# Performance work log

Measured on AMD Instinct MI355X. Metric: run time of the kernel, lower is better.

Reference implementation:

```python
import jax, jax.numpy as jnp
import numpy as np

B, S, L, D, C_ENC, H = 8, 4096, 77, 1280, 2048, 20
DH = D // H          # 64
SCALE = DH ** -0.5


def setup_inputs() -> dict:
    key = jax.random.key(0)
    ks = jax.random.split(key, 8)
    return {
        "hidden_states": jax.random.normal(ks[0], (B, S, D), jnp.float32),
        "encoder_hidden_states": jax.random.normal(ks[1], (B, L, C_ENC), jnp.float32),
        "region_state": jax.random.uniform(ks[2], (B, S, L), jnp.float32),
        "Wq": jax.random.normal(ks[3], (D, D), jnp.float32) * 0.02,
        "Wk": jax.random.normal(ks[4], (C_ENC, D), jnp.float32) * 0.02,
        "Wv": jax.random.normal(ks[5], (C_ENC, D), jnp.float32) * 0.02,
        "Wo": jax.random.normal(ks[6], (D, D), jnp.float32) * 0.02,
        "bo": jnp.zeros((D,), jnp.float32),
        "sigma": jnp.ones((1,), jnp.float32) * 14.6,
    }


def reference(hidden_states, encoder_hidden_states, region_state, Wq, Wk, Wv, Wo, bo, sigma):
    # QKV projections (dense GEMMs)
    q = (hidden_states @ Wq).reshape(B, S, H, DH)            # [B,S,H,dh]
    k = (encoder_hidden_states @ Wk).reshape(B, L, H, DH)    # [B,L,H,dh]
    v = (encoder_hidden_states @ Wv).reshape(B, L, H, DH)
    # scaled attention scores (baddbmm with beta=0 == plain scaled matmul)
    scores = jnp.einsum('bshd,blhd->bhsl', q, k) * SCALE      # [B,H,S,L]
    # region-prompt bias: weight_func(w, sigma, qk) = w * log(1 + 0.1*sigma) * qk.max()
    # repeat_interleave over heads == broadcast over the head axis
    bias = region_state * (jnp.log1p(sigma[0] * 0.1) * scores.max())  # [B,S,L]
    scores = scores + bias[:, None, :, :]
    probs = jax.nn.softmax(scores, axis=-1)
    out = jnp.einsum('bhsl,blhd->bshd', probs, v).reshape(B, S, D)
    # output projection (to_out[0]); to_out[1] is dropout (identity at eval)
    return out @ Wo + bo
```

## Files before the change

### kernel.cpp

```cpp
#include <hip/hip_runtime.h>
#include <hip/hip_bf16.h>
#include <math.h>

#define NB 8
#define NS 4096
#define NL 77
#define NLP 80
#define NLPV 96
#define ND 1280
#define NC 2048
#define NH 20
#define NDH 64
#define QK_SCALE 0.125f

typedef __attribute__((ext_vector_type(4))) float f32x4;
typedef __attribute__((ext_vector_type(8))) short bf16x8;

static __device__ __forceinline__ void gload_lds16(const void* g, void* l) {
  __builtin_amdgcn_global_load_lds(
      (const __attribute__((address_space(1))) void*)g,
      (__attribute__((address_space(3))) void*)l, 16, 0, 0);
}

#define BAR() do { asm volatile("" ::: "memory"); __builtin_amdgcn_s_barrier(); asm volatile("" ::: "memory"); } while (0)
#define LGKM0() asm volatile("s_waitcnt lgkmcnt(0)" ::: "memory")

__global__ void cvt_bf16_kern(const float* __restrict__ in,
                              __hip_bfloat16* __restrict__ out, long n)
{
  long i = ((long)blockIdx.x * blockDim.x + threadIdx.x) * 4;
  long stride = (long)gridDim.x * blockDim.x * 4;
  for (; i < n; i += stride) {
    float4 v = *reinterpret_cast<const float4*>(in + i);
    union { __hip_bfloat16 h[4]; ushort4 u; } r;
    r.h[0] = __float2bfloat16(v.x);
    r.h[1] = __float2bfloat16(v.y);
    r.h[2] = __float2bfloat16(v.z);
    r.h[3] = __float2bfloat16(v.w);
    *reinterpret_cast<ushort4*>(out + i) = r.u;
  }
}

__global__ void transpose_bf16_kern(const float* __restrict__ in,
                                    __hip_bfloat16* __restrict__ out,
                                    int rows, int cols)
{
  __shared__ float t[32][33];
  int c0 = blockIdx.x * 32, r0 = blockIdx.y * 32;
  int tx = threadIdx.x, ty = threadIdx.y;
  for (int i = ty; i < 32; i += 8) {
    int r = r0 + i, c = c0 + tx;
    t[i][tx] = (r < rows && c < cols) ? in[(long)r * cols + c] : 0.f;
  }
  __syncthreads();
  for (int i = ty; i < 32; i += 8) {
    int oc = c0 + i, orr = r0 + tx;
    if (oc < cols && orr < rows)
      out[(long)oc * rows + orr] = __float2bfloat16(t[tx][i]);
  }
}

__global__ __launch_bounds__(256)
void gemm_bt_kern(const __hip_bfloat16* __restrict__ A,
                  const __hip_bfloat16* __restrict__ Bt,
                  void* __restrict__ C, const float* __restrict__ bias,
                  int M, int N, int K, int mode)
{
  __shared__ __align__(16) __hip_bfloat16 As[128 * 32];
  __shared__ __align__(16) __hip_bfloat16 Bs[128 * 32];
  const int t = threadIdx.x;
  const int lane = t & 63;
  const int w = t >> 6;
  const int wm = w >> 1, wn = w & 1;
  const int lr = lane & 15, hi = lane >> 4, lk = hi * 8;
  const long m0 = (long)blockIdx.x * 128;
  const long n0 = (long)blockIdx.y * 128;

  f32x4 acc[4][4];
#pragma unroll
  for (int mi = 0; mi < 4; ++mi)
#pragma unroll
    for (int ni = 0; ni < 4; ++ni) acc[mi][ni] = {0.f, 0.f, 0.f, 0.f};

  for (int k0 = 0; k0 < K; k0 += 32) {
    __syncthreads();
#pragma unroll
    for (int rnd = 0; rnd < 2; ++rnd) {
      int idx = rnd * 256 + t;
      int row = idx >> 2, kpp = (idx & 3) * 8;
      long arow = m0 + row; if (arow >= M) arow = M - 1;
      gload_lds16(A + arow * K + k0 + kpp, (void*)(As + idx * 8));
      long brow = n0 + row;
      gload_lds16(Bt + brow * K + k0 + kpp, (void*)(Bs + idx * 8));
    }
    __syncthreads();

    bf16x8 af[4], bfr[4];
#pragma unroll
    for (int i = 0; i < 4; ++i) {
      af[i]  = *reinterpret_cast<const bf16x8*>(As + (wm * 64 + i * 16 + lr) * 32 + lk);
      bfr[i] = *reinterpret_cast<const bf16x8*>(Bs + (wn * 64 + i * 16 + lr) * 32 + lk);
    }
#pragma unroll
    for (int mi = 0; mi < 4; ++mi)
#pragma unroll
      for (int ni = 0; ni < 4; ++ni)
        acc[mi][ni] = __builtin_amdgcn_mfma_f32_16x16x32_bf16(af[mi], bfr[ni], acc[mi][ni], 0, 0, 0);
  }

#pragma unroll
  for (int mi = 0; mi < 4; ++mi) {
#pragma unroll
    for (int r = 0; r < 4; ++r) {
      long row = m0 + wm * 64 + mi * 16 + hi * 4 + r;
      if (row < M) {
#pragma unroll
        for (int ni = 0; ni < 4; ++ni) {
          long col = n0 + wn * 64 + ni * 16 + lr;
          if (mode == 0)
            ((__hip_bfloat16*)C)[row * N + col] = __float2bfloat16(acc[mi][ni][r]);
          else
            ((float*)C)[row * N + col] = acc[mi][ni][r] + bias[col];
        }
      }
    }
  }
}

__global__ __launch_bounds__(256, 2)
void gemm_qmax_kern(const __hip_bfloat16* __restrict__ A,
                    const __hip_bfloat16* __restrict__ Bt,
                    __hip_bfloat16* __restrict__ C,
                    const __hip_bfloat16* __restrict__ kp,
                    float* __restrict__ bmax,
                    int M, int N, int K)
{
  __shared__ __align__(16) __hip_bfloat16 sm[32768];
  char* smc = (char*)sm;

  const int t = threadIdx.x, lane = t & 63, w = t >> 6;
  const int wm = w >> 1, wn = w & 1;
  const int lr = lane & 15, hi = lane >> 4;
  const int sw = lr & 7;

  int nwg = gridDim.x;
  int cpx = nwg >> 3;
  int swz = (blockIdx.x & 7) * cpx + (blockIdx.x >> 3);
  int nxt = N >> 7;
  int mt = swz / nxt, ntile = swz - mt * nxt;
  const long m0 = (long)mt * 128, n0 = (long)ntile * 128;

  const int srow  = t >> 3;
  const int skoff = ((t & 7) ^ (srow & 7)) * 8;
  const int sdst  = t * 16;

  f32x4 acc[4][4];
#pragma unroll
  for (int mi = 0; mi < 4; ++mi)
#pragma unroll
    for (int ni = 0; ni < 4; ++ni) acc[mi][ni] = {0.f, 0.f, 0.f, 0.f};

  auto stageA = [&](int b, int kt) {
#pragma unroll
    for (int c = 0; c < 4; ++c)
      gload_lds16(A + (m0 + c * 32 + srow) * (long)K + kt * 64 + skoff,
                  (void*)(smc + b * 16384 + c * 4096 + sdst));
  };
  auto stageB = [&](int b, int kt) {
#pragma unroll
    for (int c = 0; c < 4; ++c)
      gload_lds16(Bt + (n0 + c * 32 + srow) * (long)K + kt * 64 + skoff,
                  (void*)(smc + 32768 + b * 16384 + c * 4096 + sdst));
  };

  const int NT = K >> 6;
  stageA(0, 0); stageB(0, 0);
  stageA(1, 1); stageB(1, 1);
  asm volatile("s_waitcnt vmcnt(8)" ::: "memory");
  BAR();

  for (int t2 = 0; t2 < NT; ++t2) {
    const int b = t2 & 1;
    const char* pa = smc + b * 16384;
    const char* pb = smc + 32768 + b * 16384;
    const bool pf = (t2 + 2 < NT);

    bf16x8 af[4][2], bfr[4][2];
#pragma unroll
    for (int mi = 0; mi < 4; ++mi) {
      int row = wm * 64 + mi * 16 + lr;
#pragma unroll
      for (int kk = 0; kk < 2; ++kk)
        af[mi][kk] = *reinterpret_cast<const bf16x8*>(
            pa + row * 128 + ((((kk * 4 + hi) ^ sw)) << 4));
    }
#pragma unroll
    for (int ni = 0; ni < 4; ++ni) {
      int row = wn * 64 + ni * 16 + lr;
#pragma unroll
      for (int kk = 0; kk < 2; ++kk)
        bfr[ni][kk] = *reinterpret_cast<const bf16x8*>(
            pb + row * 128 + ((((kk * 4 + hi) ^ sw)) << 4));
    }
    __builtin_amdgcn_s_setprio(1);
#pragma unroll
    for (int mi = 0; mi < 4; ++mi)
#pragma unroll
      for (int ni = 0; ni < 4; ++ni) {
        acc[mi][ni] = __builtin_amdgcn_mfma_f32_16x16x32_bf16(af[mi][0], bfr[ni][0], acc[mi][ni], 0, 0, 0);
        acc[mi][ni] = __builtin_amdgcn_mfma_f32_16x16x32_bf16(af[mi][1], bfr[ni][1], acc[mi][ni], 0, 0, 0);
      }
    __builtin_amdgcn_s_setprio(0);

    LGKM0();
    BAR();
    if (pf) { stageA(b, t2 + 2); stageB(b, t2 + 2); }
    if (pf) { asm volatile("s_waitcnt vmcnt(8)" ::: "memory"); }
    else    { asm volatile("s_waitcnt vmcnt(0)" ::: "memory"); }
    BAR();
  }

  __hip_bfloat16* qsl = (__hip_bfloat16*)smc;
#pragma unroll
  for (int mi = 0; mi < 4; ++mi)
#pragma unroll
    for (int r = 0; r < 4; ++r) {
      int rowl = wm * 64 + mi * 16 + hi * 4 + r;
      long row = m0 + rowl;
#pragma unroll
      for (int ni = 0; ni < 4; ++ni) {
        int col = wn * 64 + ni * 16 + lr;
        __hip_bfloat16 v = __float2bfloat16(acc[mi][ni][r]);
        C[row * N + n0 + col] = v;
        int bw = (col >> 3) ^ (rowl & 7);
        qsl[rowl * 128 + (bw << 3) + (col & 7)] = v;
      }
    }
  LGKM0();
  BAR();
  const int bb = (int)(m0 >> 12);
  float mx = -1e30f;
#pragma unroll
  for (int hh = 0; hh < 2; ++hh) {
    const int h = (int)(n0 >> 6) + hh;
    bf16x8 bk0[5], bk1[5];
#pragma unroll
    for (int lt = 0; lt < 5; ++lt) {
      const __hip_bfloat16* Kr = kp + ((long)(bb * NLP + lt * 16 + lr)) * ND + h * NDH + hi * 8;
      bk0[lt] = *reinterpret_cast<const bf16x8*>(Kr);
      bk1[lt] = *reinterpret_cast<const bf16x8*>(Kr + 32);
    }
#pragma unroll
    for (int su = 0; su < 2; ++su) {
      int qrow = (w * 2 + su) * 16 + lr;
      int bi0 = (hh * 8 + hi)     ^ sw;
      int bi1 = (hh * 8 + 4 + hi) ^ sw;
      bf16x8 aq0 = *reinterpret_cast<const bf16x8*>(qsl + qrow * 128 + (bi0 << 3));
      bf16x8 aq1 = *reinterpret_cast<const bf16x8*>(qsl + qrow * 128 + (bi1 << 3));
#pragma unroll
      for (int lt = 0; lt < 5; ++lt) {
        f32x4 sc = {0.f, 0.f, 0.f, 0.f};
        sc = __builtin_amdgcn_mfma_f32_16x16x32_bf16(aq0, bk0[lt], sc, 0, 0, 0);
        sc = __builtin_amdgcn_mfma_f32_16x16x32_bf16(aq1, bk1[lt], sc, 0, 0, 0);
        if ((lt < 4) || (lr < 13)) {
#pragma unroll
          for (int r = 0; r < 4; ++r) mx = fmaxf(mx, sc[r]);
        }
      }
    }
  }
#pragma unroll
  for (int k = 32; k >= 1; k >>= 1) mx = fmaxf(mx, __shfl_xor(mx, k));
  float* wmx = (float*)(smc + 32768);
  if (lane == 0) wmx[w] = mx;
  LGKM0();
  BAR();
  if (t == 0) {
    float mm = fmaxf(fmaxf(wmx[0], wmx[1]), fmaxf(wmx[2], wmx[3]));
    bmax[blockIdx.x] = mm * QK_SCALE;
  }
}

__global__ __launch_bounds__(256, 2)
void gemm_out_kern(const __hip_bfloat16* __restrict__ A,
                   const __hip_bfloat16* __restrict__ Bt,
                   float* __restrict__ C, const float* __restrict__ bias,
                   int M, int N, int K)
{
  __shared__ __align__(16) __hip_bfloat16 sm[32768];
  char* smc = (char*)sm;

  const int t = threadIdx.x, lane = t & 63, w = t >> 6;
  const int wm = w >> 1, wn = w & 1;
  const int lr = lane & 15, hi = lane >> 4;
  const int sw = lr & 7;

  int nwg = gridDim.x;
  int cpx = nwg >> 3;
  int swz = (blockIdx.x & 7) * cpx + (blockIdx.x >> 3);
  int nxt = N >> 7;
  int mt = swz / nxt, ntile = swz - mt * nxt;
  const long m0 = (long)mt * 128, n0 = (long)ntile * 128;

  const int srow  = t >> 3;
  const int skoff = ((t & 7) ^ (srow & 7)) * 8;
  const int sdst  = t * 16;

  f32x4 acc[4][4];
#pragma unroll
  for (int mi = 0; mi < 4; ++mi)
#pragma unroll
    for (int ni = 0; ni < 4; ++ni) acc[mi][ni] = {0.f, 0.f, 0.f, 0.f};

  auto stageA = [&](int b, int kt) {
#pragma unroll
    for (int c = 0; c < 4; ++c)
      gload_lds16(A + (m0 + c * 32 + srow) * (long)K + kt * 64 + skoff,
                  (void*)(smc + b * 16384 + c * 4096 + sdst));
  };
  auto stageB = [&](int b, int kt) {
#pragma unroll
    for (int c = 0; c < 4; ++c)
      gload_lds16(Bt + (n0 + c * 32 + srow) * (long)K + kt * 64 + skoff,
                  (void*)(smc + 32768 + b * 16384 + c * 4096 + sdst));
  };

  const int NT = K >> 6;
  stageA(0, 0); stageB(0, 0);
  stageA(1, 1); stageB(1, 1);
  asm volatile("s_waitcnt vmcnt(8)" ::: "memory");
  BAR();

  for (int t2 = 0; t2 < NT; ++t2) {
    const int b = t2 & 1;
    const char* pa = smc + b * 16384;
    const char* pb = smc + 32768 + b * 16384;
    const bool pf = (t2 + 2 < NT);

    bf16x8 af[4][2], bfr[4][2];
#pragma unroll
    for (int mi = 0; mi < 4; ++mi) {
      int row = wm * 64 + mi * 16 + lr;
#pragma unroll
      for (int kk = 0; kk < 2; ++kk)
        af[mi][kk] = *reinterpret_cast<const bf16x8*>(
            pa + row * 128 + ((((kk * 4 + hi) ^ sw)) << 4));
    }
#pragma unroll
    for (int ni = 0; ni < 4; ++ni) {
      int row = wn * 64 + ni * 16 + lr;
#pragma unroll
      for (int kk = 0; kk < 2; ++kk)
        bfr[ni][kk] = *reinterpret_cast<const bf16x8*>(
            pb + row * 128 + ((((kk * 4 + hi) ^ sw)) << 4));
    }
    __builtin_amdgcn_s_setprio(1);
#pragma unroll
    for (int mi = 0; mi < 4; ++mi)
#pragma unroll
      for (int ni = 0; ni < 4; ++ni) {
        acc[mi][ni] = __builtin_amdgcn_mfma_f32_16x16x32_bf16(af[mi][0], bfr[ni][0], acc[mi][ni], 0, 0, 0);
        acc[mi][ni] = __builtin_amdgcn_mfma_f32_16x16x32_bf16(af[mi][1], bfr[ni][1], acc[mi][ni], 0, 0, 0);
      }
    __builtin_amdgcn_s_setprio(0);

    LGKM0();
    BAR();
    if (pf) { stageA(b, t2 + 2); stageB(b, t2 + 2); }
    if (pf) { asm volatile("s_waitcnt vmcnt(8)" ::: "memory"); }
    else    { asm volatile("s_waitcnt vmcnt(0)" ::: "memory"); }
    BAR();
  }

  float bv[4];
#pragma unroll
  for (int ni = 0; ni < 4; ++ni) bv[ni] = bias[n0 + wn * 64 + ni * 16 + lr];
#pragma unroll
  for (int mi = 0; mi < 4; ++mi)
#pragma unroll
    for (int r = 0; r < 4; ++r) {
      long row = m0 + wm * 64 + mi * 16 + hi * 4 + r;
#pragma unroll
      for (int ni = 0; ni < 4; ++ni) {
        long col = n0 + wn * 64 + ni * 16 + lr;
        C[row * N + col] = acc[mi][ni][r] + bv[ni];
      }
    }
}

__global__ void repack_kv_kern(const __hip_bfloat16* __restrict__ kvc,
                               __hip_bfloat16* __restrict__ kp,
                               __hip_bfloat16* __restrict__ vt)
{
  int idx = blockIdx.x * 256 + threadIdx.x;
  const __hip_bfloat16 z = __float2bfloat16(0.f);
  if (idx < NB * NLP * ND) {
    int d = idx % ND;
    int l = (idx / ND) % NLP;
    int b = idx / (ND * NLP);
    kp[idx] = (l < NL) ? kvc[((long)(b * NL + l)) * 2560 + d] : z;
  }
  if (idx < NB * NH * NDH * NLPV) {
    int l  = idx % NLPV;
    int dh = (idx / NLPV) % NDH;
    int h  = (idx / (NLPV * NDH)) % NH;
    int b  = idx / (NLPV * NDH * NH);
    vt[idx] = (l < NL) ? kvc[((long)(b * NL + l)) * 2560 + ND + h * NDH + dh] : z;
  }
}

__global__ void reduce_max_kern(const float* __restrict__ bm, int n,
                                const float* __restrict__ sigma,
                                float* __restrict__ cb)
{
  __shared__ float sm[256];
  float m = -1e30f;
  for (int i = threadIdx.x; i < n; i += 256) m = fmaxf(m, bm[i]);
  sm[threadIdx.x] = m;
  __syncthreads();
  for (int s = 128; s > 0; s >>= 1) {
    if (threadIdx.x < (unsigned)s) sm[threadIdx.x] = fmaxf(sm[threadIdx.x], sm[threadIdx.x + s]);
    __syncthreads();
  }
  if (threadIdx.x == 0) cb[0] = log1pf(sigma[0] * 0.1f) * sm[0];
}

__global__ __launch_bounds__(256)
void attn_kern(const __hip_bfloat16* __restrict__ qb,
               const __hip_bfloat16* __restrict__ kp,
               const __hip_bfloat16* __restrict__ vt,
               const float* __restrict__ rs,
               const float* __restrict__ cb,
               __hip_bfloat16* __restrict__ ao_out)
{
  __shared__ __align__(16) __hip_bfloat16 pl[4][16][NLPV];
  int t = threadIdx.x, lane = t & 63, wi = t >> 6;
  int b = blockIdx.z, h = blockIdx.y;
  int lr = lane & 15, hi = lane >> 4, lk = hi * 8;
  const float c = cb[0];

  bf16x8 bk[5][2];
#pragma unroll
  for (int lt = 0; lt < 5; ++lt) {
    const __hip_bfloat16* Kr = kp + ((long)(b * NLP + lt * 16 + lr)) * ND + h * NDH + lk;
    bk[lt][0] = *reinterpret_cast<const bf16x8*>(Kr);
    bk[lt][1] = *reinterpret_cast<const bf16x8*>(Kr + 32);
  }
#pragma unroll
  for (int r = 0; r < 4; ++r)
    pl[wi][hi * 4 + r][80 + lr] = __float2bfloat16(0.f);

  const __hip_bfloat16* Vb = vt + ((long)((b * NH + h) * NDH)) * NLPV;

#pragma unroll
  for (int st = 0; st < 4; ++st) {
    int s0 = blockIdx.x * 256 + wi * 64 + st * 16;
    const __hip_bfloat16* Qp = qb + ((long)(b * NS + s0 + lr)) * ND + h * NDH + lk;
    bf16x8 aq0 = *reinterpret_cast<const bf16x8*>(Qp);
    bf16x8 aq1 = *reinterpret_cast<const bf16x8*>(Qp + 32);

    f32x4 sc[5];
#pragma unroll
    for (int lt = 0; lt < 5; ++lt) {
      f32x4 z = {0.f, 0.f, 0.f, 0.f};
      z = __builtin_amdgcn_mfma_f32_16x16x32_bf16(aq0, bk[lt][0], z, 0, 0, 0);
      sc[lt] = __builtin_amdgcn_mfma_f32_16x16x32_bf16(aq1, bk[lt][1], z, 0, 0, 0);
    }

    float sv[5][4];
    float pm[4] = {-1e30f, -1e30f, -1e30f, -1e30f};
#pragma unroll
    for (int lt = 0; lt < 5; ++lt) {
      int l = lt * 16 + lr;
#pragma unroll
      for (int r = 0; r < 4; ++r) {
        if (l < NL) {
          int srow = s0 + hi * 4 + r;
          float v = sc[lt][r] * QK_SCALE + rs[((long)(b * NS + srow)) * NL + l] * c;
          sv[lt][r] = v;
          pm[r] = fmaxf(pm[r], v);
        } else {
          sv[lt][r] = -1e30f;
        }
      }
    }
#pragma unroll
    for (int r = 0; r < 4; ++r)
#pragma unroll
      for (int k = 8; k >= 1; k >>= 1) pm[r] = fmaxf(pm[r], __shfl_xor(pm[r], k));

    float p[5][4];
    float psum[4] = {0.f, 0.f, 0.f, 0.f};
#pragma unroll
    for (int lt = 0; lt < 5; ++lt) {
      int l = lt * 16 + lr;
#pragma unroll
      for (int r = 0; r < 4; ++r) {
        float e = (l < NL) ? __expf(sv[lt][r] - pm[r]) : 0.f;
        p[lt][r] = e;
        psum[r] += e;
      }
    }
#pragma unroll
    for (int r = 0; r < 4; ++r)
#pragma unroll
      for (int k = 8; k >= 1; k >>= 1) psum[r] += __shfl_xor(psum[r], k);
    float rinv[4];
#pragma unroll
    for (int r = 0; r < 4; ++r) rinv[r] = 1.f / psum[r];

    LGKM0();

#pragma unroll
    for (int lt = 0; lt < 5; ++lt)
#pragma unroll
      for (int r = 0; r < 4; ++r)
        pl[wi][hi * 4 + r][lt * 16 + lr] = __float2bfloat16(p[lt][r]);

    LGKM0();

    f32x4 ao[4];
#pragma unroll
    for (int nt = 0; nt < 4; ++nt) ao[nt] = {0.f, 0.f, 0.f, 0.f};
#pragma unroll
    for (int ks = 0; ks < 3; ++ks) {
      bf16x8 pa = *reinterpret_cast<const bf16x8*>(&pl[wi][lr][ks * 32 + lk]);
#pragma unroll
      for (int nt = 0; nt < 4; ++nt) {
        bf16x8 bv = *reinterpret_cast<const bf16x8*>(Vb + ((long)(nt * 16 + lr)) * NLPV + ks * 32 + lk);
        ao[nt] = __builtin_amdgcn_mfma_f32_16x16x32_bf16(pa, bv, ao[nt], 0, 0, 0);
      }
    }

#pragma unroll
    for (int nt = 0; nt < 4; ++nt)
#pragma unroll
      for (int r = 0; r < 4; ++r) {
        int srow = s0 + hi * 4 + r;
        ao_out[((long)(b * NS + srow)) * ND + h * NDH + nt * 16 + lr] =
            __float2bfloat16(ao[nt][r] * rinv[r]);
      }
  }
}

extern "C" void kernel_launch(void* const* d_in, const int* in_sizes, int n_in,
                              void* d_out, int out_size, void* d_ws, size_t ws_size,
                              hipStream_t stream)
{
  const float* hs    = (const float*)d_in[0];
  const float* ehs   = (const float*)d_in[1];
  const float* rs    = (const float*)d_in[2];
  const float* Wq    = (const float*)d_in[3];
  const float* Wk    = (const float*)d_in[4];
  const float* Wv    = (const float*)d_in[5];
  const float* Wo    = (const float*)d_in[6];
  const float* bo    = (const float*)d_in[7];
  const float* sigma = (const float*)d_in[8];
  float* out = (float*)d_out;

  char* ws = (char*)d_ws;
  size_t off = 0;
  auto alloc = [&](size_t bytes) {
    void* p = ws + off;
    off = (off + bytes + 255) & ~(size_t)255;
    return p;
  };
  __hip_bfloat16* hsb  = (__hip_bfloat16*)alloc((size_t)NB * NS * ND * 2);
  __hip_bfloat16* qb   = (__hip_bfloat16*)alloc((size_t)NB * NS * ND * 2);
  __hip_bfloat16* wqt  = (__hip_bfloat16*)alloc((size_t)ND * ND * 2);
  __hip_bfloat16* wkvt = (__hip_bfloat16*)alloc((size_t)2560 * NC * 2);
  __hip_bfloat16* wot  = (__hip_bfloat16*)alloc((size_t)ND * ND * 2);
  __hip_bfloat16* ehsb = (__hip_bfloat16*)alloc((size_t)NB * NL * NC * 2);
  __hip_bfloat16* kvc  = (__hip_bfloat16*)alloc((size_t)NB * NL * 2560 * 2);
  __hip_bfloat16* kp   = (__hip_bfloat16*)alloc((size_t)NB * NLP * ND * 2);
  __hip_bfloat16* vt   = (__hip_bfloat16*)alloc((size_t)NB * NH * NDH * NLPV * 2);
  float* bmax = (float*)alloc(10240 * 4);
  float* cb   = (float*)alloc(256);

  cvt_bf16_kern<<<2048, 256, 0, stream>>>(hs, hsb, (long)NB * NS * ND);
  cvt_bf16_kern<<<512, 256, 0, stream>>>(ehs, ehsb, (long)NB * NL * NC);

  transpose_bf16_kern<<<dim3(40, 40), dim3(32, 8), 0, stream>>>(Wq, wqt, ND, ND);
  transpose_bf16_kern<<<dim3(40, 64), dim3(32, 8), 0, stream>>>(Wk, wkvt, NC, ND);
  transpose_bf16_kern<<<dim3(40, 64), dim3(32, 8), 0, stream>>>(Wv, wkvt + (size_t)ND * NC, NC, ND);
  transpose_bf16_kern<<<dim3(40, 40), dim3(32, 8), 0, stream>>>(Wo, wot, ND, ND);

  gemm_bt_kern<<<dim3(5, 20), 256, 0, stream>>>(ehsb, wkvt, kvc, nullptr, NB * NL, 2560, NC, 0);
  repack_kv_kern<<<3840, 256, 0, stream>>>(kvc, kp, vt);

  gemm_qmax_kern<<<2560, 256, 0, stream>>>(hsb, wqt, qb, kp, bmax, NB * NS, ND, ND);

  reduce_max_kern<<<1, 256, 0, stream>>>(bmax, 2560, sigma, cb);

  attn_kern<<<dim3(16, NH, NB), 256, 0, stream>>>(qb, kp, vt, rs, cb, hsb);

  gemm_out_kern<<<2560, 256, 0, stream>>>(hsb, wot, out, bo, NB * NS, ND, ND);
}
```

Before: 490.4 us.

## Restructure attention grid to loop over heads and stage region bias in LDS

The attention kernel now assigns each block 64 query rows of one batch and loops over all 20 heads, rather than one head with 256 rows. The region_state tile is loaded once into shared memory, premultiplied by the bias constant, and reused across heads, so the bias is no longer re-read from global memory 20 times. In exchange, K fragments are reloaded from global memory each head iteration, and the grid is smaller, with more serial work per block.

```diff
diff --git a/kernel.cpp b/kernel.cpp
--- a/kernel.cpp
+++ b/kernel.cpp
@@ -433,38 +433,41 @@
                const float* __restrict__ cb,
                __hip_bfloat16* __restrict__ ao_out)
 {
+  __shared__ __align__(16) float rsl[64][80];
   __shared__ __align__(16) __hip_bfloat16 pl[4][16][NLPV];
   int t = threadIdx.x, lane = t & 63, wi = t >> 6;
-  int b = blockIdx.z, h = blockIdx.y;
+  int b = blockIdx.y;
+  int s0 = blockIdx.x * 64;
   int lr = lane & 15, hi = lane >> 4, lk = hi * 8;
   const float c = cb[0];
 
-  bf16x8 bk[5][2];
-#pragma unroll
-  for (int lt = 0; lt < 5; ++lt) {
-    const __hip_bfloat16* Kr = kp + ((long)(b * NLP + lt * 16 + lr)) * ND + h * NDH + lk;
-    bk[lt][0] = *reinterpret_cast<const bf16x8*>(Kr);
-    bk[lt][1] = *reinterpret_cast<const bf16x8*>(Kr + 32);
+  for (int i = t; i < 64 * NL; i += 256) {
+    int rr = i / NL, cc = i - rr * NL;
+    rsl[rr][cc] = rs[((long)(b * NS + s0 + rr)) * NL + cc] * c;
   }
 #pragma unroll
   for (int r = 0; r < 4; ++r)
     pl[wi][hi * 4 + r][80 + lr] = __float2bfloat16(0.f);
-
-  const __hip_bfloat16* Vb = vt + ((long)((b * NH + h) * NDH)) * NLPV;
-
-#pragma unroll
-  for (int st = 0; st < 4; ++st) {
-    int s0 = blockIdx.x * 256 + wi * 64 + st * 16;
-    const __hip_bfloat16* Qp = qb + ((long)(b * NS + s0 + lr)) * ND + h * NDH + lk;
+  __syncthreads();
+
+  const int rw = wi * 16;
+  const __hip_bfloat16* Qrow = qb + ((long)(b * NS + s0 + rw + lr)) * ND;
+  const __hip_bfloat16* Krow = kp + ((long)(b * NLP + lr)) * ND;
+
+  for (int h = 0; h < NH; ++h) {
+    const __hip_bfloat16* Qp = Qrow + h * NDH + lk;
     bf16x8 aq0 = *reinterpret_cast<const bf16x8*>(Qp);
     bf16x8 aq1 = *reinterpret_cast<const bf16x8*>(Qp + 32);
 
     f32x4 sc[5];
 #pragma unroll
     for (int lt = 0; lt < 5; ++lt) {
+      const __hip_bfloat16* Kr = Krow + (long)lt * 16 * ND + h * NDH + lk;
+      bf16x8 bk0 = *reinterpret_cast<const bf16x8*>(Kr);
+      bf16x8 bk1 = *reinterpret_cast<const bf16x8*>(Kr + 32);
       f32x4 z = {0.f, 0.f, 0.f, 0.f};
-      z = __builtin_amdgcn_mfma_f32_16x16x32_bf16(aq0, bk[lt][0], z, 0, 0, 0);
-      sc[lt] = __builtin_amdgcn_mfma_f32_16x16x32_bf16(aq1, bk[lt][1], z, 0, 0, 0);
+      z = __builtin_amdgcn_mfma_f32_16x16x32_bf16(aq0, bk0, z, 0, 0, 0);
+      sc[lt] = __builtin_amdgcn_mfma_f32_16x16x32_bf16(aq1, bk1, z, 0, 0, 0);
     }
 
     float sv[5][4];
@@ -475,8 +478,7 @@
 #pragma unroll
       for (int r = 0; r < 4; ++r) {
         if (l < NL) {
-          int srow = s0 + hi * 4 + r;
-          float v = sc[lt][r] * QK_SCALE + rs[((long)(b * NS + srow)) * NL + l] * c;
+          float v = sc[lt][r] * QK_SCALE + rsl[rw + hi * 4 + r][l];
           sv[lt][r] = v;
           pm[r] = fmaxf(pm[r], v);
         } else {
@@ -522,6 +524,7 @@
     f32x4 ao[4];
 #pragma unroll
     for (int nt = 0; nt < 4; ++nt) ao[nt] = {0.f, 0.f, 0.f, 0.f};
+    const __hip_bfloat16* Vb = vt + ((long)((b * NH + h) * NDH)) * NLPV;
 #pragma unroll
     for (int ks = 0; ks < 3; ++ks) {
       bf16x8 pa = *reinterpret_cast<const bf16x8*>(&pl[wi][lr][ks * 32 + lk]);
@@ -536,7 +539,7 @@
     for (int nt = 0; nt < 4; ++nt)
 #pragma unroll
       for (int r = 0; r < 4; ++r) {
-        int srow = s0 + hi * 4 + r;
+        int srow = s0 + rw + hi * 4 + r;
         ao_out[((long)(b * NS + srow)) * ND + h * NDH + nt * 16 + lr] =
             __float2bfloat16(ao[nt][r] * rinv[r]);
       }
@@ -592,7 +595,7 @@
 
   reduce_max_kern<<<1, 256, 0, stream>>>(bmax, 2560, sigma, cb);
 
-  attn_kern<<<dim3(16, NH, NB), 256, 0, stream>>>(qb, kp, vt, rs, cb, hsb);
+  attn_kern<<<dim3(NS / 64, NB), 256, 0, stream>>>(qb, kp, vt, rs, cb, hsb);
 
   gemm_out_kern<<<2560, 256, 0, stream>>>(hsb, wot, out, bo, NB * NS, ND, ND);
 }
```

New measurement: 484.5 us. No clear change (-1.2%).
